# Optimization experiments

Measured on AMD Instinct MI355X. Metric: run time of the kernel, lower is better.

Reference implementation:

```python
import jax, jax.numpy as jnp
import numpy as np

B, T, H, DK, DV, HID, C = 2, 4096, 16, 128, 128, 2048, 64  # chunk size 64 (fla default)
EPS = 1e-5


def setup_inputs() -> dict:
    key = jax.random.key(0)
    ks = jax.random.split(key, 8)
    s = 0.02
    return dict(
        hidden_ab=jax.random.normal(ks[0], (B, T, HID), jnp.float32),
        hidden_g=jax.random.normal(ks[1], (B, T, HID), jnp.float32),
        q=jax.random.normal(ks[2], (B, T, H, DK), jnp.float32),
        k=jax.random.normal(ks[3], (B, T, H, DK), jnp.float32),
        v=jax.random.normal(ks[4], (B, T, H, DV), jnp.float32),
        Wb=jax.random.normal(ks[5], (HID, H), jnp.float32) * s,
        Wg=jax.random.normal(ks[6], (HID, H), jnp.float32) * s,
        o_norm_w=jnp.ones((DV,), jnp.float32),
        o_proj_w=jax.random.normal(ks[7], (H, DV, DK), jnp.float32) * s,
    )


def _l2norm(x):
    return x * jax.lax.rsqrt(jnp.sum(x * x, -1, keepdims=True) + 1e-6)


def reference(hidden_ab, hidden_g, q, k, v, Wb, Wg, o_norm_w, o_proj_w):
    # beta gate per head (training path: sigmoid(b_proj(hidden_ab)))
    beta = jax.nn.sigmoid(hidden_ab @ Wb)  # [B,T,H]
    # qk_norm == 'l2' -> l2 normalization inside the kernel, q scaled by dk^-0.5
    q = _l2norm(q)
    k = _l2norm(k)
    scale = DK ** -0.5
    N = T // C

    def toc(x, d):  # [B,T,H,d] -> [N,B,H,C,d]
        return x.reshape(B, N, C, H, d).transpose(1, 0, 3, 2, 4)

    qc = toc(q * scale, DK)
    kc = toc(k, DK)
    vc = toc(v, DV)
    bc = beta.reshape(B, N, C, H).transpose(1, 0, 3, 2)  # [N,B,H,C]

    k_beta = kc * bc[..., None]
    v_beta = vc * bc[..., None]

    # intra-chunk UT transform: Tm = (I + strict_lower(k_beta k^T))^{-1}
    Lm = jnp.tril(jnp.einsum('nbhik,nbhjk->nbhij', k_beta, kc), -1)  # [N,B,H,C,C]
    eye = jnp.eye(C, dtype=q.dtype)
    Tm = jax.scipy.linalg.solve_triangular(eye + Lm, jnp.broadcast_to(eye, Lm.shape), lower=True)
    u = Tm @ v_beta   # [N,B,H,C,DV]
    w = Tm @ k_beta   # [N,B,H,C,DK]
    attn = jnp.tril(jnp.einsum('nbhik,nbhjk->nbhij', qc, kc))  # causal intra-chunk scores

    def step(S, ins):  # S: [B,H,DK,DV] carried state
        qn, kn, an, un, wn = ins
        vi = un - wn @ S                                   # corrected values
        on = qn @ S + an @ vi                              # inter + intra chunk output
        S = S + jnp.einsum('bhck,bhcv->bhkv', kn, vi)      # state update
        return S, on

    S0 = jnp.zeros((B, H, DK, DV), q.dtype)
    _, o = jax.lax.scan(step, S0, (qc, kc, attn, u, w))    # o: [N,B,H,C,DV]
    o = o.transpose(1, 0, 3, 2, 4).reshape(B, T, H, DV)

    # FusedRMSNormSwishGate with per-head scalar gate broadcast over DV
    g = hidden_g @ Wg  # [B,T,H]
    o = o * jax.lax.rsqrt(jnp.mean(o * o, -1, keepdims=True) + EPS) * o_norm_w
    o = o * (g * jax.nn.sigmoid(g))[..., None]

    # GroupLinear: per-head DV -> head_dim projection, then flatten heads
    out = jnp.einsum('bthv,hvd->bthd', o, o_proj_w).reshape(B, T, H * DK)
    return out
```

## Files before the change

kernel.cpp:

```cpp
#include <hip/hip_runtime.h>
#include <hip/hip_bf16.h>

#define BB 2
#define TT 4096
#define HH 16
#define DKk 128
#define DVv 128
#define HIDD 2048
#define CC 64
#define NN 64
#define GG 8
#define QSCALE 0.08838834764831845f

static __device__ __forceinline__ unsigned short f2bf(float f) {
  unsigned u = __float_as_uint(f);
  u += 0x7fffu + ((u >> 16) & 1u);
  return (unsigned short)(u >> 16);
}
static __device__ __forceinline__ float bf2f(unsigned short s) {
  return __uint_as_float(((unsigned)s) << 16);
}

static __device__ __forceinline__ void barrier_lds_only() {
  asm volatile("s_waitcnt lgkmcnt(0)\n\ts_barrier" ::: "memory");
}

typedef short bf8 __attribute__((ext_vector_type(8)));
typedef float f4 __attribute__((ext_vector_type(4)));

__global__ __launch_bounds__(256) void k0_wt(
    const float* __restrict__ Wb, const float* __restrict__ Wg,
    unsigned short* __restrict__ Wtb, unsigned short* __restrict__ Wtg) {
  int blk = blockIdx.x;
  const float* W = (blk < 8) ? Wb : Wg;
  unsigned short* Wt = (blk < 8) ? Wtb : Wtg;
  int k0 = (blk & 7) * 256;
  int tid = threadIdx.x;
  __shared__ unsigned short st[16][272];
  const float* p = W + (size_t)(k0 + tid) * HH;
#pragma unroll
  for (int h4 = 0; h4 < 4; h4++) {
    float4 x = *(const float4*)(p + h4 * 4);
    st[h4 * 4 + 0][tid] = f2bf(x.x);
    st[h4 * 4 + 1][tid] = f2bf(x.y);
    st[h4 * 4 + 2][tid] = f2bf(x.z);
    st[h4 * 4 + 3][tid] = f2bf(x.w);
  }
  __syncthreads();
  int h = tid >> 4, c = (tid & 15) << 4;
#pragma unroll
  for (int j = 0; j < 16; j++)
    Wt[(size_t)h * HIDD + k0 + c + j] = st[h][c + j];
}

__global__ __launch_bounds__(256) void k1_beta_g(
    const float* __restrict__ hab, const float* __restrict__ hg,
    const unsigned short* __restrict__ Wtb, const unsigned short* __restrict__ Wtg,
    float* __restrict__ beta, float* __restrict__ graw) {
  int tile = blockIdx.x;
  int tid = threadIdx.x;
  int w = tid >> 6, lane = tid & 63;
  int proj = w >> 1, ks = w & 1;
  int n16 = lane & 15, qd = lane >> 4;
  const float* hid = proj ? hg : hab;
  const unsigned short* Wt = proj ? Wtg : Wtb;
  size_t rowbase = (size_t)(tile * 16 + n16) * HIDD;
  int k0 = ks * 1024;

  f4 acc = {0.f, 0.f, 0.f, 0.f};
  for (int s = 0; s < 32; s++) {
    int kk = k0 + s * 32 + qd * 8;
    const float* hp = hid + rowbase + kk;
    float4 h0 = *(const float4*)hp;
    float4 h1 = *(const float4*)(hp + 4);
    bf8 a;
    a[0] = (short)f2bf(h0.x); a[1] = (short)f2bf(h0.y);
    a[2] = (short)f2bf(h0.z); a[3] = (short)f2bf(h0.w);
    a[4] = (short)f2bf(h1.x); a[5] = (short)f2bf(h1.y);
    a[6] = (short)f2bf(h1.z); a[7] = (short)f2bf(h1.w);
    bf8 b = *(const bf8*)&Wt[(size_t)n16 * HIDD + kk];
    acc = __builtin_amdgcn_mfma_f32_16x16x32_bf16(a, b, acc, 0, 0, 0);
  }

  __shared__ float red[2][16][17];
  if (ks == 1) {
#pragma unroll
    for (int r = 0; r < 4; r++) red[proj][qd * 4 + r][n16] = acc[r];
  }
  __syncthreads();
  if (ks == 0) {
#pragma unroll
    for (int r = 0; r < 4; r++) {
      float s = acc[r] + red[proj][qd * 4 + r][n16];
      size_t t = (size_t)(tile * 16 + qd * 4 + r) * HH + n16;
      if (proj == 0) beta[t] = 1.f / (1.f + expf(-s));
      else           graw[t] = s;
    }
  }
}

__global__ __launch_bounds__(256) void k2_l2norm(
    const float* __restrict__ q, const float* __restrict__ k,
    unsigned short* __restrict__ qn, unsigned short* __restrict__ kn) {
  int lane = threadIdx.x & 63, wave = threadIdx.x >> 6;
  for (int u = 0; u < 2; u++) {
    int vec = blockIdx.x * 8 + wave * 2 + u;
    size_t off = (size_t)vec * 64 + lane;
    float2 q2 = ((const float2*)q)[off];
    float2 k2 = ((const float2*)k)[off];
    float sq = q2.x * q2.x + q2.y * q2.y;
    float sk = k2.x * k2.x + k2.y * k2.y;
#pragma unroll
    for (int m = 32; m; m >>= 1) { sq += __shfl_xor(sq, m); sk += __shfl_xor(sk, m); }
    float rq = rsqrtf(sq + 1e-6f) * QSCALE;
    float rk = rsqrtf(sk + 1e-6f);
    unsigned pq = (unsigned)f2bf(q2.x * rq) | ((unsigned)f2bf(q2.y * rq) << 16);
    unsigned pk = (unsigned)f2bf(k2.x * rk) | ((unsigned)f2bf(k2.y * rk) << 16);
    ((unsigned*)qn)[off] = pq;
    ((unsigned*)kn)[off] = pk;
  }
}

#define SW 72
#define K3_M0R 8704
#define K3_M0T 13312
#define K3_M1R 17920
#define K3_M1T 22528
#define K3_TB  27136
#define K3_ARENA 31744

__global__ __launch_bounds__(256) void k3_chunk(
    const unsigned short* __restrict__ qn, const unsigned short* __restrict__ kn,
    const float* __restrict__ beta,
    unsigned short* __restrict__ ATg, unsigned short* __restrict__ Ktg) {
  int cid = blockIdx.x;
  int n = cid & (NN - 1);
  int bh = cid / NN;
  int h = bh & (HH - 1);
  int b = bh / HH;
  int tid = threadIdx.x;
  int w = tid >> 6;
  int lane = tid & 63;
  int n16 = lane & 15;
  int qd = lane >> 4;
  int r0 = w * 16;

  __shared__ __align__(16) unsigned short arena[K3_ARENA];
  __shared__ float sb[CC];
  unsigned short* sk = arena;
  unsigned short* sq = arena + 8704;

  int t0 = n * CC;
#pragma unroll
  for (int p = 0; p < 4; p++) {
    int id = p * 256 + tid, row = id >> 4, c8 = (id & 15) << 3;
    size_t g = ((size_t)((b * TT + t0 + row) * HH + h)) * DKk + c8;
    *(uint4*)&sk[row * 136 + c8] = *(const uint4*)(kn + g);
    *(uint4*)&sq[row * 136 + c8] = *(const uint4*)(qn + g);
  }
  if (tid < CC) sb[tid] = beta[(size_t)((b * TT + t0 + tid) * HH + h)];
  __syncthreads();

  f4 at[4], mk[4];
#pragma unroll
  for (int ct = 0; ct < 4; ct++) { at[ct] = (f4){0,0,0,0}; mk[ct] = (f4){0,0,0,0}; }
#pragma unroll
  for (int s = 0; s < 4; s++) {
    bf8 aq = *(const bf8*)&sq[(r0 + n16) * 136 + s * 32 + qd * 8];
    bf8 ak = *(const bf8*)&sk[(r0 + n16) * 136 + s * 32 + qd * 8];
#pragma unroll
    for (int ct = 0; ct < 4; ct++) {
      bf8 bk = *(const bf8*)&sk[(ct * 16 + n16) * 136 + s * 32 + qd * 8];
      at[ct] = __builtin_amdgcn_mfma_f32_16x16x32_bf16(aq, bk, at[ct], 0, 0, 0);
      mk[ct] = __builtin_amdgcn_mfma_f32_16x16x32_bf16(ak, bk, mk[ct], 0, 0, 0);
    }
  }

  f4 tf[4];
  float mpv[4][4];
#pragma unroll
  for (int ct = 0; ct < 4; ct++) {
#pragma unroll
    for (int r = 0; r < 4; r++) {
      int i = r0 + qd * 4 + r, j = ct * 16 + n16;
      at[ct][r] = (j <= i) ? at[ct][r] : 0.f;
      float mp = (j < i) ? -sb[i] * mk[ct][r] : 0.f;
      mpv[ct][r] = mp;
      tf[ct][r] = (i == j) ? 1.f : mp;
    }
  }
  __syncthreads();

#pragma unroll
  for (int ct = 0; ct < 4; ct++) {
#pragma unroll
    for (int r = 0; r < 4; r++) {
      int i = r0 + qd * 4 + r, j = ct * 16 + n16;
      unsigned short hm = f2bf(mpv[ct][r]);
      arena[K3_M0R + i * SW + j] = hm;
      arena[K3_M0T + j * SW + i] = hm;
      arena[K3_TB + j * SW + i] = f2bf(tf[ct][r]);
    }
  }
  __syncthreads();

  int p = 0;
  for (int it = 1; it <= 5; it++) {
    int mrp = p ? K3_M1R : K3_M0R, mtp = p ? K3_M1T : K3_M0T;
    int mrn = p ? K3_M0R : K3_M1R, mtn = p ? K3_M0T : K3_M1T;
    f4 nr[4];
#pragma unroll
    for (int ct = 0; ct < 4; ct++) nr[ct] = (f4){0,0,0,0};
#pragma unroll
    for (int s = 0; s < 2; s++) {
      bf8 a = *(const bf8*)&arena[mrp + (r0 + n16) * SW + s * 32 + qd * 8];
#pragma unroll
      for (int ct = 0; ct < 4; ct++) {
        bf8 bb = *(const bf8*)&arena[mtp + (ct * 16 + n16) * SW + s * 32 + qd * 8];
        nr[ct] = __builtin_amdgcn_mfma_f32_16x16x32_bf16(a, bb, nr[ct], 0, 0, 0);
      }
    }
#pragma unroll
    for (int ct = 0; ct < 4; ct++) {
#pragma unroll
      for (int r = 0; r < 4; r++) {
        int i = r0 + qd * 4 + r, j = ct * 16 + n16;
        unsigned short hm = f2bf(nr[ct][r]);
        arena[mrn + i * SW + j] = hm;
        arena[mtn + j * SW + i] = hm;
      }
    }
    __syncthreads();

#pragma unroll
    for (int s = 0; s < 2; s++) {
      bf8 a = *(const bf8*)&arena[mrn + (r0 + n16) * SW + s * 32 + qd * 8];
#pragma unroll
      for (int ct = 0; ct < 4; ct++) {
        bf8 bb = *(const bf8*)&arena[K3_TB + (ct * 16 + n16) * SW + s * 32 + qd * 8];
        tf[ct] = __builtin_amdgcn_mfma_f32_16x16x32_bf16(a, bb, tf[ct], 0, 0, 0);
      }
    }
    __syncthreads();

    if (it < 5) {
#pragma unroll
      for (int ct = 0; ct < 4; ct++) {
#pragma unroll
        for (int r = 0; r < 4; r++) {
          int i = r0 + qd * 4 + r, j = ct * 16 + n16;
          arena[K3_TB + j * SW + i] = f2bf(tf[ct][r]);
        }
      }
    }
    p = 1 - p;
  }

#pragma unroll
  for (int ct = 0; ct < 4; ct++) {
#pragma unroll
    for (int r = 0; r < 4; r++) {
      int i = r0 + qd * 4 + r, j = ct * 16 + n16;
      arena[K3_M0R + i * SW + j] = f2bf(at[ct][r]);
      arena[K3_TB + j * SW + i] = f2bf(tf[ct][r]);
    }
  }
  __syncthreads();

  {
    f4 ac[4];
#pragma unroll
    for (int ct = 0; ct < 4; ct++) ac[ct] = (f4){0,0,0,0};
#pragma unroll
    for (int s = 0; s < 2; s++) {
      bf8 a = *(const bf8*)&arena[K3_M0R + (r0 + n16) * SW + s * 32 + qd * 8];
#pragma unroll
      for (int ct = 0; ct < 4; ct++) {
        bf8 bb = *(const bf8*)&arena[K3_TB + (ct * 16 + n16) * SW + s * 32 + qd * 8];
        ac[ct] = __builtin_amdgcn_mfma_f32_16x16x32_bf16(a, bb, ac[ct], 0, 0, 0);
      }
    }
    size_t abase = (size_t)cid * (CC * CC);
#pragma unroll
    for (int ct = 0; ct < 4; ct++)
#pragma unroll
      for (int r = 0; r < 4; r++)
        ATg[abase + (r0 + qd * 4 + r) * CC + ct * 16 + n16] = f2bf(ac[ct][r]);
  }

  {
    size_t kbase = (size_t)cid * (DKk * CC);
#pragma unroll
    for (int t = 0; t < 2; t++) {
      int dkt = w * 32 + t * 16;
      f4 ac[4];
#pragma unroll
      for (int ct = 0; ct < 4; ct++) ac[ct] = (f4){0,0,0,0};
#pragma unroll
      for (int s = 0; s < 2; s++) {
        bf8 a;
#pragma unroll
        for (int jj = 0; jj < 8; jj++)
          a[jj] = (short)sk[(s * 32 + qd * 8 + jj) * 136 + dkt + n16];
#pragma unroll
        for (int ct = 0; ct < 4; ct++) {
          bf8 bb = *(const bf8*)&arena[K3_TB + (ct * 16 + n16) * SW + s * 32 + qd * 8];
          ac[ct] = __builtin_amdgcn_mfma_f32_16x16x32_bf16(a, bb, ac[ct], 0, 0, 0);
        }
      }
#pragma unroll
      for (int ct = 0; ct < 4; ct++)
#pragma unroll
        for (int r = 0; r < 4; r++)
          Ktg[kbase + (dkt + qd * 4 + r) * CC + ct * 16 + n16] = f2bf(ac[ct][r]);
    }
  }
}

__global__ __launch_bounds__(256) void k4_scan(
    const unsigned short* __restrict__ qn, const unsigned short* __restrict__ kn,
    const float* __restrict__ v, const float* __restrict__ beta,
    const unsigned short* __restrict__ ATg, const unsigned short* __restrict__ Ktg,
    float* __restrict__ o) {
  int bi = blockIdx.x;
  int jg = bi >> 5;
  int bh = bi & 31;
  int h = bh & (HH - 1);
  int b = bh >> 4;
  int tid = threadIdx.x;
  int j0 = jg * 16;
  int w = tid >> 6;
  int lane = tid & 63;
  int n16 = lane & 15;
  int qd = lane >> 4;
  int r0 = w * 16;
  int dkbase = w * 32;

  __shared__ __align__(16) unsigned short sk[CC * 136];
  __shared__ __align__(16) unsigned short sq[CC * 136];
  __shared__ __align__(16) unsigned short sSb[16 * 136];
  __shared__ __align__(16) unsigned short sAT[2][CC * SW];
  __shared__ __align__(16) unsigned short sKt[2][DKk * SW];
  __shared__ __align__(16) unsigned short sxT[2][16 * SW];
  __shared__ float sb[CC];

  f4 S0 = {0.f, 0.f, 0.f, 0.f}, S1 = {0.f, 0.f, 0.f, 0.f};
  for (int i = tid; i < 16 * 136; i += 256) sSb[i] = 0;

  int bhBase = (b * HH + h) * NN;

  uint4 pk[4], pq[4], pat[2], pkt[4];
  float4 pv;
  float pb = 0.f;

  {
#pragma unroll
    for (int p = 0; p < 4; p++) {
      int id = p * 256 + tid, row = id >> 4, c8 = (id & 15) << 3;
      size_t g = ((size_t)((b * TT + row) * HH + h)) * DKk + c8;
      pk[p] = *(const uint4*)(kn + g);
      pq[p] = *(const uint4*)(qn + g);
    }
    size_t cb = (size_t)bhBase * (CC * CC);
#pragma unroll
    for (int p = 0; p < 2; p++) {
      int id = p * 256 + tid, row = id >> 3, c8 = (id & 7) << 3;
      pat[p] = *(const uint4*)(ATg + cb + row * CC + c8);
    }
    size_t kb = (size_t)bhBase * (DKk * CC);
#pragma unroll
    for (int p = 0; p < 4; p++) {
      int id = p * 256 + tid, row = id >> 3, c8 = (id & 7) << 3;
      pkt[p] = *(const uint4*)(Ktg + kb + row * CC + c8);
    }
    {
      int c = tid >> 2, c4 = (tid & 3) << 2;
      pv = *(const float4*)(v + ((size_t)((b * TT + c) * HH + h)) * DVv + j0 + c4);
    }
    if (tid < CC) pb = beta[(size_t)((b * TT + tid) * HH + h)];
  }

  for (int n = 0; n < NN; n++) {
    int t0 = n * CC;
    unsigned short* xT = sxT[n & 1];
    unsigned short* aT = sAT[n & 1];
    unsigned short* kT = sKt[n & 1];

#pragma unroll
    for (int p = 0; p < 4; p++) {
      int id = p * 256 + tid, row = id >> 4, c8 = (id & 15) << 3;
      *(uint4*)&sk[row * 136 + c8] = pk[p];
      *(uint4*)&sq[row * 136 + c8] = pq[p];
    }
#pragma unroll
    for (int p = 0; p < 2; p++) {
      int id = p * 256 + tid, row = id >> 3, c8 = (id & 7) << 3;
      *(uint4*)&aT[row * SW + c8] = pat[p];
    }
#pragma unroll
    for (int p = 0; p < 4; p++) {
      int id = p * 256 + tid, row = id >> 3, c8 = (id & 7) << 3;
      *(uint4*)&kT[row * SW + c8] = pkt[p];
    }
    {
      int c = tid >> 2, c4 = (tid & 3) << 2;
      xT[(c4 + 0) * SW + c] = f2bf(pv.x);
      xT[(c4 + 1) * SW + c] = f2bf(pv.y);
      xT[(c4 + 2) * SW + c] = f2bf(pv.z);
      xT[(c4 + 3) * SW + c] = f2bf(pv.w);
    }
    if (tid < CC) sb[tid] = pb;
    barrier_lds_only();

    if (n + 1 < NN) {
      int t0n = t0 + CC;
#pragma unroll
      for (int p = 0; p < 4; p++) {
        int id = p * 256 + tid, row = id >> 4, c8 = (id & 15) << 3;
        size_t g = ((size_t)((b * TT + t0n + row) * HH + h)) * DKk + c8;
        pk[p] = *(const uint4*)(kn + g);
        pq[p] = *(const uint4*)(qn + g);
      }
      size_t cb = (size_t)(bhBase + n + 1) * (CC * CC);
#pragma unroll
      for (int p = 0; p < 2; p++) {
        int id = p * 256 + tid, row = id >> 3, c8 = (id & 7) << 3;
        pat[p] = *(const uint4*)(ATg + cb + row * CC + c8);
      }
      size_t kb = (size_t)(bhBase + n + 1) * (DKk * CC);
#pragma unroll
      for (int p = 0; p < 4; p++) {
        int id = p * 256 + tid, row = id >> 3, c8 = (id & 7) << 3;
        pkt[p] = *(const uint4*)(Ktg + kb + row * CC + c8);
      }
      {
        int c = tid >> 2, c4 = (tid & 3) << 2;
        pv = *(const float4*)(v + ((size_t)((b * TT + t0n + c) * HH + h)) * DVv + j0 + c4);
      }
      if (tid < CC) pb = beta[(size_t)((b * TT + t0n + tid) * HH + h)];
    }

    f4 oacc;
    {
      bf8 bS0 = *(const bf8*)&sSb[n16 * 136 + 0 * 32 + qd * 8];
      bf8 bS1 = *(const bf8*)&sSb[n16 * 136 + 1 * 32 + qd * 8];
      bf8 bS2 = *(const bf8*)&sSb[n16 * 136 + 2 * 32 + qd * 8];
      bf8 bS3 = *(const bf8*)&sSb[n16 * 136 + 3 * 32 + qd * 8];
      bf8 aK0 = *(const bf8*)&sk[(r0 + n16) * 136 + 0 * 32 + qd * 8];
      bf8 aK1 = *(const bf8*)&sk[(r0 + n16) * 136 + 1 * 32 + qd * 8];
      bf8 aK2 = *(const bf8*)&sk[(r0 + n16) * 136 + 2 * 32 + qd * 8];
      bf8 aK3 = *(const bf8*)&sk[(r0 + n16) * 136 + 3 * 32 + qd * 8];
      bf8 aQ0 = *(const bf8*)&sq[(r0 + n16) * 136 + 0 * 32 + qd * 8];
      bf8 aQ1 = *(const bf8*)&sq[(r0 + n16) * 136 + 1 * 32 + qd * 8];
      bf8 aQ2 = *(const bf8*)&sq[(r0 + n16) * 136 + 2 * 32 + qd * 8];
      bf8 aQ3 = *(const bf8*)&sq[(r0 + n16) * 136 + 3 * 32 + qd * 8];
      f4 xa = {0.f, 0.f, 0.f, 0.f}, xc = {0.f, 0.f, 0.f, 0.f};
      f4 oa = {0.f, 0.f, 0.f, 0.f}, ob = {0.f, 0.f, 0.f, 0.f};
      xa = __builtin_amdgcn_mfma_f32_16x16x32_bf16(aK0, bS0, xa, 0, 0, 0);
      xa = __builtin_amdgcn_mfma_f32_16x16x32_bf16(aK1, bS1, xa, 0, 0, 0);
      xc = __builtin_amdgcn_mfma_f32_16x16x32_bf16(aK2, bS2, xc, 0, 0, 0);
      xc = __builtin_amdgcn_mfma_f32_16x16x32_bf16(aK3, bS3, xc, 0, 0, 0);
      oa = __builtin_amdgcn_mfma_f32_16x16x32_bf16(aQ0, bS0, oa, 0, 0, 0);
      oa = __builtin_amdgcn_mfma_f32_16x16x32_bf16(aQ1, bS1, oa, 0, 0, 0);
      ob = __builtin_amdgcn_mfma_f32_16x16x32_bf16(aQ2, bS2, ob, 0, 0, 0);
      ob = __builtin_amdgcn_mfma_f32_16x16x32_bf16(aQ3, bS3, ob, 0, 0, 0);
      oacc = oa + ob;
#pragma unroll
      for (int r = 0; r < 4; r++) {
        int c = r0 + qd * 4 + r;
        float vv = bf2f(xT[n16 * SW + c]);
        xT[n16 * SW + c] = f2bf(sb[c] * (vv - (xa[r] + xc[r])));
      }
    }
    barrier_lds_only();

    {
      bf8 bx0 = *(const bf8*)&xT[n16 * SW + 0 * 32 + qd * 8];
      bf8 bx1 = *(const bf8*)&xT[n16 * SW + 1 * 32 + qd * 8];
      bf8 aA0 = *(const bf8*)&aT[(r0 + n16) * SW + 0 * 32 + qd * 8];
      bf8 aA1 = *(const bf8*)&aT[(r0 + n16) * SW + 1 * 32 + qd * 8];
      oacc = __builtin_amdgcn_mfma_f32_16x16x32_bf16(aA0, bx0, oacc, 0, 0, 0);
      oacc = __builtin_amdgcn_mfma_f32_16x16x32_bf16(aA1, bx1, oacc, 0, 0, 0);
#pragma unroll
      for (int r = 0; r < 4; r++) {
        int c = r0 + qd * 4 + r;
        o[((size_t)((b * TT + t0 + c) * HH + h)) * DVv + j0 + n16] = oacc[r];
      }
      bf8 aT0 = *(const bf8*)&kT[(dkbase + n16) * SW + 0 * 32 + qd * 8];
      bf8 aT1 = *(const bf8*)&kT[(dkbase + n16) * SW + 1 * 32 + qd * 8];
      S0 = __builtin_amdgcn_mfma_f32_16x16x32_bf16(aT0, bx0, S0, 0, 0, 0);
      S0 = __builtin_amdgcn_mfma_f32_16x16x32_bf16(aT1, bx1, S0, 0, 0, 0);
      bf8 aT2 = *(const bf8*)&kT[(dkbase + 16 + n16) * SW + 0 * 32 + qd * 8];
      bf8 aT3 = *(const bf8*)&kT[(dkbase + 16 + n16) * SW + 1 * 32 + qd * 8];
      S1 = __builtin_amdgcn_mfma_f32_16x16x32_bf16(aT2, bx0, S1, 0, 0, 0);
      S1 = __builtin_amdgcn_mfma_f32_16x16x32_bf16(aT3, bx1, S1, 0, 0, 0);
#pragma unroll
      for (int r = 0; r < 4; r++) {
        sSb[n16 * 136 + dkbase + qd * 4 + r] = f2bf(S0[r]);
        sSb[n16 * 136 + dkbase + 16 + qd * 4 + r] = f2bf(S1[r]);
      }
    }
  }
}

__global__ __launch_bounds__(256) void k5_out(
    const float* __restrict__ graw, const float* __restrict__ onw,
    const float* __restrict__ opw, float* __restrict__ out) {
  int bi = blockIdx.x;
  int h = bi & (HH - 1);
  int tt = (bi >> 4) & 127;
  int b = bi >> 11;
  int t0 = tt * 32;
  int tid = threadIdx.x;

  __shared__ __align__(16) unsigned short sP[DVv * DKk];
  __shared__ __align__(16) float so[32 * 129];
  __shared__ float smul[32];
  __shared__ float snw[DVv];

  const float* P = opw + (size_t)h * DVv * DKk;
  for (int r = 0; r < 16; r++) {
    int idx4 = r * 256 + tid;
    float4 pvv = *(const float4*)(P + ((size_t)idx4 << 2));
    unsigned p0 = (unsigned)f2bf(pvv.x) | ((unsigned)f2bf(pvv.y) << 16);
    unsigned p1 = (unsigned)f2bf(pvv.z) | ((unsigned)f2bf(pvv.w) << 16);
    *(uint2*)&sP[idx4 << 2] = make_uint2(p0, p1);
  }
  for (int r = 0; r < 16; r++) {
    int idx = r * 256 + tid;
    int t = idx >> 7, d = idx & 127;
    so[t * 129 + d] = out[((size_t)((b * TT + t0 + t) * HH + h)) * DVv + d];
  }
  if (tid < DVv) snw[tid] = onw[tid];
  __syncthreads();

  {
    int t = tid >> 3, l8 = tid & 7;
    float ss = 0.f;
    for (int j = 0; j < 16; j++) { float x = so[t * 129 + l8 + (j << 3)]; ss += x * x; }
    ss += __shfl_down(ss, 4, 8);
    ss += __shfl_down(ss, 2, 8);
    ss += __shfl_down(ss, 1, 8);
    if (l8 == 0) {
      float rms = rsqrtf(ss * (1.f / 128.f) + 1e-5f);
      float gv = graw[(size_t)((b * TT + t0 + t) * HH + h)];
      float sig = 1.f / (1.f + expf(-gv));
      smul[t] = rms * gv * sig;
    }
  }
  __syncthreads();
  for (int r = 0; r < 16; r++) {
    int idx = r * 256 + tid;
    int t = idx >> 7, d = idx & 127;
    so[t * 129 + d] *= smul[t] * snw[d];
  }
  __syncthreads();

  {
    int ttile = tid >> 5;
    int dt = tid & 31;
    int tb = ttile << 2;
    int d0 = dt << 2;
    float acc[4][4];
#pragma unroll
    for (int a = 0; a < 4; a++)
#pragma unroll
      for (int e = 0; e < 4; e++) acc[a][e] = 0.f;
    for (int vv = 0; vv < DVv; vv++) {
      uint2 u = *(const uint2*)&sP[vv * DKk + d0];
      float p0 = __uint_as_float(u.x << 16);
      float p1 = __uint_as_float(u.x & 0xffff0000u);
      float p2 = __uint_as_float(u.y << 16);
      float p3 = __uint_as_float(u.y & 0xffff0000u);
#pragma unroll
      for (int a = 0; a < 4; a++) {
        float ov = so[(tb + a) * 129 + vv];
        acc[a][0] += ov * p0; acc[a][1] += ov * p1; acc[a][2] += ov * p2; acc[a][3] += ov * p3;
      }
    }
#pragma unroll
    for (int a = 0; a < 4; a++) {
      size_t go = ((size_t)((b * TT + t0 + tb + a) * HH + h)) * DKk + d0;
      float4 r; r.x = acc[a][0]; r.y = acc[a][1]; r.z = acc[a][2]; r.w = acc[a][3];
      *(float4*)(out + go) = r;
    }
  }
}

extern "C" void kernel_launch(void* const* d_in, const int* in_sizes, int n_in,
                              void* d_out, int out_size, void* d_ws, size_t ws_size,
                              hipStream_t stream) {
  (void)in_sizes; (void)n_in; (void)out_size; (void)ws_size;
  const float* hab = (const float*)d_in[0];
  const float* hg  = (const float*)d_in[1];
  const float* q   = (const float*)d_in[2];
  const float* k   = (const float*)d_in[3];
  const float* v   = (const float*)d_in[4];
  const float* Wb  = (const float*)d_in[5];
  const float* Wg  = (const float*)d_in[6];
  const float* onw = (const float*)d_in[7];
  const float* opw = (const float*)d_in[8];
  float* out = (float*)d_out;

  char* ws = (char*)d_ws;
  float* beta          = (float*)(ws);
  float* graw          = (float*)(ws + 524288);
  unsigned short* qn   = (unsigned short*)(ws + 1048576);
  unsigned short* kn   = (unsigned short*)(ws + 34603008);
  unsigned short* ATg  = (unsigned short*)(ws + 68157440);
  unsigned short* Ktg  = (unsigned short*)(ws + 84934656);
  unsigned short* Wtb  = (unsigned short*)(ws + 118489088);
  unsigned short* Wtg  = (unsigned short*)(ws + 118554624);

  hipLaunchKernelGGL(k0_wt, dim3(16), dim3(256), 0, stream,
                     Wb, Wg, Wtb, Wtg);
  hipLaunchKernelGGL(k1_beta_g, dim3(TT * BB / 16), dim3(256), 0, stream,
                     hab, hg, Wtb, Wtg, beta, graw);
  hipLaunchKernelGGL(k2_l2norm, dim3(BB * TT * HH / 8), dim3(256), 0, stream,
                     q, k, qn, kn);
  hipLaunchKernelGGL(k3_chunk, dim3(BB * HH * NN), dim3(256), 0, stream,
                     qn, kn, beta, ATg, Ktg);
  hipLaunchKernelGGL(k4_scan, dim3(BB * HH * GG), dim3(256), 0, stream,
                     qn, kn, v, beta, ATg, Ktg, out);
  hipLaunchKernelGGL(k5_out, dim3(BB * (TT / 32) * HH), dim3(256), 0, stream,
                     graw, onw, opw, out);
}
```

Measured before the change: 611.0 us.

## Load scan operands directly into MFMA registers and use MFMA for output projection

The scan kernel stops staging k, q, AT and Kt chunks through shared memory. Each lane now prefetches its own MFMA fragments straight from global memory into registers, double-buffered across two chunk bodies, which removes most LDS traffic and barriers on the serial per-chunk path. The output-projection kernel swaps its scalar FMA loop for bf16 MFMA, using a weight matrix that a new small kernel pre-transposes to bf16. The cost is higher register pressure in the scan, now pinned at one block per CU, plus an extra launch and workspace buffer.

```diff
diff --git a/kernel.cpp b/kernel.cpp
--- a/kernel.cpp
+++ b/kernel.cpp
@@ -51,6 +51,33 @@
 #pragma unroll
   for (int j = 0; j < 16; j++)
     Wt[(size_t)h * HIDD + k0 + c + j] = st[h][c + j];
+}
+
+__global__ __launch_bounds__(256) void k0p_pt(
+    const float* __restrict__ opw, unsigned short* __restrict__ Ppt) {
+  int h = blockIdx.x;
+  int tid = threadIdx.x;
+  __shared__ unsigned short sp[128 * 132];
+  const float* P = opw + (size_t)h * (DVv * DKk);
+  for (int it = 0; it < 16; it++) {
+    int idx = it * 256 + tid;
+    int vv = idx >> 5, d4 = (idx & 31) << 2;
+    float4 x = *(const float4*)(P + vv * 128 + d4);
+    sp[vv * 132 + d4 + 0] = f2bf(x.x);
+    sp[vv * 132 + d4 + 1] = f2bf(x.y);
+    sp[vv * 132 + d4 + 2] = f2bf(x.z);
+    sp[vv * 132 + d4 + 3] = f2bf(x.w);
+  }
+  __syncthreads();
+  unsigned short* dst = Ppt + (size_t)h * (DVv * DKk);
+  for (int it = 0; it < 8; it++) {
+    int idx = it * 256 + tid;
+    int d = idx >> 4, v8 = (idx & 15) << 3;
+    unsigned short tmp[8];
+#pragma unroll
+    for (int j = 0; j < 8; j++) tmp[j] = sp[(v8 + j) * 132 + d];
+    *(uint4*)&dst[d * 128 + v8] = *(uint4*)tmp;
+  }
 }
 
 __global__ __launch_bounds__(256) void k1_beta_g(
@@ -317,7 +344,112 @@
   }
 }
 
-__global__ __launch_bounds__(256) void k4_scan(
+struct K4Frag {
+  bf8 k0, k1, k2, k3;
+  bf8 q0, q1, q2, q3;
+  bf8 a0, a1;
+  bf8 t0, t1, t2, t3;
+  float4 vv;
+  float b0, b1, b2, b3;
+};
+
+static __device__ __forceinline__ void k4_prefetch(
+    K4Frag& F, int n,
+    const unsigned short* knb, const unsigned short* qnb,
+    const unsigned short* atb, const unsigned short* ktb,
+    const float* vb, const float* bb) {
+  const unsigned short* kp = knb + (size_t)n * (CC * HH * DKk);
+  F.k0 = *(const bf8*)(kp);
+  F.k1 = *(const bf8*)(kp + 32);
+  F.k2 = *(const bf8*)(kp + 64);
+  F.k3 = *(const bf8*)(kp + 96);
+  const unsigned short* qp = qnb + (size_t)n * (CC * HH * DKk);
+  F.q0 = *(const bf8*)(qp);
+  F.q1 = *(const bf8*)(qp + 32);
+  F.q2 = *(const bf8*)(qp + 64);
+  F.q3 = *(const bf8*)(qp + 96);
+  const unsigned short* ap = atb + (size_t)n * (CC * CC);
+  F.a0 = *(const bf8*)(ap);
+  F.a1 = *(const bf8*)(ap + 32);
+  const unsigned short* tp = ktb + (size_t)n * (DKk * CC);
+  F.t0 = *(const bf8*)(tp);
+  F.t1 = *(const bf8*)(tp + 32);
+  F.t2 = *(const bf8*)(tp + 1024);
+  F.t3 = *(const bf8*)(tp + 1024 + 32);
+  F.vv = *(const float4*)(vb + (size_t)n * (CC * HH * DVv));
+  const float* bp = bb + (size_t)n * (CC * HH);
+  F.b0 = bp[0]; F.b1 = bp[HH]; F.b2 = bp[2 * HH]; F.b3 = bp[3 * HH];
+}
+
+static __device__ __forceinline__ void k4_body(
+    const K4Frag& F, K4Frag& FN, int n, bool pf,
+    f4& S0, f4& S1,
+    unsigned short* xT, unsigned short* sSb,
+    float* opn,
+    int n16, int qd, int r0, int dkbase,
+    const unsigned short* knb, const unsigned short* qnb,
+    const unsigned short* atb, const unsigned short* ktb,
+    const float* vb, const float* bb) {
+  if (pf) k4_prefetch(FN, n + 1, knb, qnb, atb, ktb, vb, bb);
+
+  {
+    int col = r0 + n16;
+    xT[(qd * 4 + 0) * SW + col] = f2bf(F.vv.x);
+    xT[(qd * 4 + 1) * SW + col] = f2bf(F.vv.y);
+    xT[(qd * 4 + 2) * SW + col] = f2bf(F.vv.z);
+    xT[(qd * 4 + 3) * SW + col] = f2bf(F.vv.w);
+  }
+  barrier_lds_only();
+
+  f4 oacc;
+  {
+    bf8 bS0 = *(const bf8*)&sSb[n16 * 136 + 0 + qd * 8];
+    bf8 bS1 = *(const bf8*)&sSb[n16 * 136 + 32 + qd * 8];
+    bf8 bS2 = *(const bf8*)&sSb[n16 * 136 + 64 + qd * 8];
+    bf8 bS3 = *(const bf8*)&sSb[n16 * 136 + 96 + qd * 8];
+    f4 xa = {0.f, 0.f, 0.f, 0.f}, xc = {0.f, 0.f, 0.f, 0.f};
+    f4 oa = {0.f, 0.f, 0.f, 0.f}, ob = {0.f, 0.f, 0.f, 0.f};
+    xa = __builtin_amdgcn_mfma_f32_16x16x32_bf16(F.k0, bS0, xa, 0, 0, 0);
+    xa = __builtin_amdgcn_mfma_f32_16x16x32_bf16(F.k1, bS1, xa, 0, 0, 0);
+    xc = __builtin_amdgcn_mfma_f32_16x16x32_bf16(F.k2, bS2, xc, 0, 0, 0);
+    xc = __builtin_amdgcn_mfma_f32_16x16x32_bf16(F.k3, bS3, xc, 0, 0, 0);
+    oa = __builtin_amdgcn_mfma_f32_16x16x32_bf16(F.q0, bS0, oa, 0, 0, 0);
+    oa = __builtin_amdgcn_mfma_f32_16x16x32_bf16(F.q1, bS1, oa, 0, 0, 0);
+    ob = __builtin_amdgcn_mfma_f32_16x16x32_bf16(F.q2, bS2, ob, 0, 0, 0);
+    ob = __builtin_amdgcn_mfma_f32_16x16x32_bf16(F.q3, bS3, ob, 0, 0, 0);
+    oacc = oa + ob;
+    float bv[4] = {F.b0, F.b1, F.b2, F.b3};
+#pragma unroll
+    for (int r = 0; r < 4; r++) {
+      int c = r0 + qd * 4 + r;
+      float vval = bf2f(xT[n16 * SW + c]);
+      xT[n16 * SW + c] = f2bf(bv[r] * (vval - (xa[r] + xc[r])));
+    }
+  }
+  barrier_lds_only();
+
+  {
+    bf8 bx0 = *(const bf8*)&xT[n16 * SW + qd * 8];
+    bf8 bx1 = *(const bf8*)&xT[n16 * SW + 32 + qd * 8];
+    oacc = __builtin_amdgcn_mfma_f32_16x16x32_bf16(F.a0, bx0, oacc, 0, 0, 0);
+    oacc = __builtin_amdgcn_mfma_f32_16x16x32_bf16(F.a1, bx1, oacc, 0, 0, 0);
+#pragma unroll
+    for (int r = 0; r < 4; r++) opn[r * (HH * DVv)] = oacc[r];
+    S0 = __builtin_amdgcn_mfma_f32_16x16x32_bf16(F.t0, bx0, S0, 0, 0, 0);
+    S0 = __builtin_amdgcn_mfma_f32_16x16x32_bf16(F.t1, bx1, S0, 0, 0, 0);
+    S1 = __builtin_amdgcn_mfma_f32_16x16x32_bf16(F.t2, bx0, S1, 0, 0, 0);
+    S1 = __builtin_amdgcn_mfma_f32_16x16x32_bf16(F.t3, bx1, S1, 0, 0, 0);
+    uint2 w0, w1;
+    w0.x = (unsigned)f2bf(S0[0]) | ((unsigned)f2bf(S0[1]) << 16);
+    w0.y = (unsigned)f2bf(S0[2]) | ((unsigned)f2bf(S0[3]) << 16);
+    w1.x = (unsigned)f2bf(S1[0]) | ((unsigned)f2bf(S1[1]) << 16);
+    w1.y = (unsigned)f2bf(S1[2]) | ((unsigned)f2bf(S1[3]) << 16);
+    *(uint2*)&sSb[n16 * 136 + dkbase + qd * 4] = w0;
+    *(uint2*)&sSb[n16 * 136 + dkbase + 16 + qd * 4] = w1;
+  }
+}
+
+__global__ __launch_bounds__(256, 1) void k4_scan(
     const unsigned short* __restrict__ qn, const unsigned short* __restrict__ kn,
     const float* __restrict__ v, const float* __restrict__ beta,
     const unsigned short* __restrict__ ATg, const unsigned short* __restrict__ Ktg,
@@ -336,200 +468,60 @@
   int r0 = w * 16;
   int dkbase = w * 32;
 
-  __shared__ __align__(16) unsigned short sk[CC * 136];
-  __shared__ __align__(16) unsigned short sq[CC * 136];
   __shared__ __align__(16) unsigned short sSb[16 * 136];
-  __shared__ __align__(16) unsigned short sAT[2][CC * SW];
-  __shared__ __align__(16) unsigned short sKt[2][DKk * SW];
   __shared__ __align__(16) unsigned short sxT[2][16 * SW];
-  __shared__ float sb[CC];
 
   f4 S0 = {0.f, 0.f, 0.f, 0.f}, S1 = {0.f, 0.f, 0.f, 0.f};
   for (int i = tid; i < 16 * 136; i += 256) sSb[i] = 0;
 
-  int bhBase = (b * HH + h) * NN;
-
-  uint4 pk[4], pq[4], pat[2], pkt[4];
-  float4 pv;
-  float pb = 0.f;
-
-  {
-#pragma unroll
-    for (int p = 0; p < 4; p++) {
-      int id = p * 256 + tid, row = id >> 4, c8 = (id & 15) << 3;
-      size_t g = ((size_t)((b * TT + row) * HH + h)) * DKk + c8;
-      pk[p] = *(const uint4*)(kn + g);
-      pq[p] = *(const uint4*)(qn + g);
-    }
-    size_t cb = (size_t)bhBase * (CC * CC);
-#pragma unroll
-    for (int p = 0; p < 2; p++) {
-      int id = p * 256 + tid, row = id >> 3, c8 = (id & 7) << 3;
-      pat[p] = *(const uint4*)(ATg + cb + row * CC + c8);
-    }
-    size_t kb = (size_t)bhBase * (DKk * CC);
-#pragma unroll
-    for (int p = 0; p < 4; p++) {
-      int id = p * 256 + tid, row = id >> 3, c8 = (id & 7) << 3;
-      pkt[p] = *(const uint4*)(Ktg + kb + row * CC + c8);
-    }
-    {
-      int c = tid >> 2, c4 = (tid & 3) << 2;
-      pv = *(const float4*)(v + ((size_t)((b * TT + c) * HH + h)) * DVv + j0 + c4);
-    }
-    if (tid < CC) pb = beta[(size_t)((b * TT + tid) * HH + h)];
-  }
-
-  for (int n = 0; n < NN; n++) {
-    int t0 = n * CC;
-    unsigned short* xT = sxT[n & 1];
-    unsigned short* aT = sAT[n & 1];
-    unsigned short* kT = sKt[n & 1];
-
-#pragma unroll
-    for (int p = 0; p < 4; p++) {
-      int id = p * 256 + tid, row = id >> 4, c8 = (id & 15) << 3;
-      *(uint4*)&sk[row * 136 + c8] = pk[p];
-      *(uint4*)&sq[row * 136 + c8] = pq[p];
-    }
-#pragma unroll
-    for (int p = 0; p < 2; p++) {
-      int id = p * 256 + tid, row = id >> 3, c8 = (id & 7) << 3;
-      *(uint4*)&aT[row * SW + c8] = pat[p];
-    }
-#pragma unroll
-    for (int p = 0; p < 4; p++) {
-      int id = p * 256 + tid, row = id >> 3, c8 = (id & 7) << 3;
-      *(uint4*)&kT[row * SW + c8] = pkt[p];
-    }
-    {
-      int c = tid >> 2, c4 = (tid & 3) << 2;
-      xT[(c4 + 0) * SW + c] = f2bf(pv.x);
-      xT[(c4 + 1) * SW + c] = f2bf(pv.y);
-      xT[(c4 + 2) * SW + c] = f2bf(pv.z);
-      xT[(c4 + 3) * SW + c] = f2bf(pv.w);
-    }
-    if (tid < CC) sb[tid] = pb;
-    barrier_lds_only();
-
-    if (n + 1 < NN) {
-      int t0n = t0 + CC;
-#pragma unroll
-      for (int p = 0; p < 4; p++) {
-        int id = p * 256 + tid, row = id >> 4, c8 = (id & 15) << 3;
-        size_t g = ((size_t)((b * TT + t0n + row) * HH + h)) * DKk + c8;
-        pk[p] = *(const uint4*)(kn + g);
-        pq[p] = *(const uint4*)(qn + g);
-      }
-      size_t cb = (size_t)(bhBase + n + 1) * (CC * CC);
-#pragma unroll
-      for (int p = 0; p < 2; p++) {
-        int id = p * 256 + tid, row = id >> 3, c8 = (id & 7) << 3;
-        pat[p] = *(const uint4*)(ATg + cb + row * CC + c8);
-      }
-      size_t kb = (size_t)(bhBase + n + 1) * (DKk * CC);
-#pragma unroll
-      for (int p = 0; p < 4; p++) {
-        int id = p * 256 + tid, row = id >> 3, c8 = (id & 7) << 3;
-        pkt[p] = *(const uint4*)(Ktg + kb + row * CC + c8);
-      }
-      {
-        int c = tid >> 2, c4 = (tid & 3) << 2;
-        pv = *(const float4*)(v + ((size_t)((b * TT + t0n + c) * HH + h)) * DVv + j0 + c4);
-      }
-      if (tid < CC) pb = beta[(size_t)((b * TT + t0n + tid) * HH + h)];
-    }
-
-    f4 oacc;
-    {
-      bf8 bS0 = *(const bf8*)&sSb[n16 * 136 + 0 * 32 + qd * 8];
-      bf8 bS1 = *(const bf8*)&sSb[n16 * 136 + 1 * 32 + qd * 8];
-      bf8 bS2 = *(const bf8*)&sSb[n16 * 136 + 2 * 32 + qd * 8];
-      bf8 bS3 = *(const bf8*)&sSb[n16 * 136 + 3 * 32 + qd * 8];
-      bf8 aK0 = *(const bf8*)&sk[(r0 + n16) * 136 + 0 * 32 + qd * 8];
-      bf8 aK1 = *(const bf8*)&sk[(r0 + n16) * 136 + 1 * 32 + qd * 8];
-      bf8 aK2 = *(const bf8*)&sk[(r0 + n16) * 136 + 2 * 32 + qd * 8];
-      bf8 aK3 = *(const bf8*)&sk[(r0 + n16) * 136 + 3 * 32 + qd * 8];
-      bf8 aQ0 = *(const bf8*)&sq[(r0 + n16) * 136 + 0 * 32 + qd * 8];
-      bf8 aQ1 = *(const bf8*)&sq[(r0 + n16) * 136 + 1 * 32 + qd * 8];
-      bf8 aQ2 = *(const bf8*)&sq[(r0 + n16) * 136 + 2 * 32 + qd * 8];
-      bf8 aQ3 = *(const bf8*)&sq[(r0 + n16) * 136 + 3 * 32 + qd * 8];
-      f4 xa = {0.f, 0.f, 0.f, 0.f}, xc = {0.f, 0.f, 0.f, 0.f};
-      f4 oa = {0.f, 0.f, 0.f, 0.f}, ob = {0.f, 0.f, 0.f, 0.f};
-      xa = __builtin_amdgcn_mfma_f32_16x16x32_bf16(aK0, bS0, xa, 0, 0, 0);
-      xa = __builtin_amdgcn_mfma_f32_16x16x32_bf16(aK1, bS1, xa, 0, 0, 0);
-      xc = __builtin_amdgcn_mfma_f32_16x16x32_bf16(aK2, bS2, xc, 0, 0, 0);
-      xc = __builtin_amdgcn_mfma_f32_16x16x32_bf16(aK3, bS3, xc, 0, 0, 0);
-      oa = __builtin_amdgcn_mfma_f32_16x16x32_bf16(aQ0, bS0, oa, 0, 0, 0);
-      oa = __builtin_amdgcn_mfma_f32_16x16x32_bf16(aQ1, bS1, oa, 0, 0, 0);
-      ob = __builtin_amdgcn_mfma_f32_16x16x32_bf16(aQ2, bS2, ob, 0, 0, 0);
-      ob = __builtin_amdgcn_mfma_f32_16x16x32_bf16(aQ3, bS3, ob, 0, 0, 0);
-      oacc = oa + ob;
-#pragma unroll
-      for (int r = 0; r < 4; r++) {
-        int c = r0 + qd * 4 + r;
-        float vv = bf2f(xT[n16 * SW + c]);
-        xT[n16 * SW + c] = f2bf(sb[c] * (vv - (xa[r] + xc[r])));
-      }
-    }
-    barrier_lds_only();
-
-    {
-      bf8 bx0 = *(const bf8*)&xT[n16 * SW + 0 * 32 + qd * 8];
-      bf8 bx1 = *(const bf8*)&xT[n16 * SW + 1 * 32 + qd * 8];
-      bf8 aA0 = *(const bf8*)&aT[(r0 + n16) * SW + 0 * 32 + qd * 8];
-      bf8 aA1 = *(const bf8*)&aT[(r0 + n16) * SW + 1 * 32 + qd * 8];
-      oacc = __builtin_amdgcn_mfma_f32_16x16x32_bf16(aA0, bx0, oacc, 0, 0, 0);
-      oacc = __builtin_amdgcn_mfma_f32_16x16x32_bf16(aA1, bx1, oacc, 0, 0, 0);
-#pragma unroll
-      for (int r = 0; r < 4; r++) {
-        int c = r0 + qd * 4 + r;
-        o[((size_t)((b * TT + t0 + c) * HH + h)) * DVv + j0 + n16] = oacc[r];
-      }
-      bf8 aT0 = *(const bf8*)&kT[(dkbase + n16) * SW + 0 * 32 + qd * 8];
-      bf8 aT1 = *(const bf8*)&kT[(dkbase + n16) * SW + 1 * 32 + qd * 8];
-      S0 = __builtin_amdgcn_mfma_f32_16x16x32_bf16(aT0, bx0, S0, 0, 0, 0);
-      S0 = __builtin_amdgcn_mfma_f32_16x16x32_bf16(aT1, bx1, S0, 0, 0, 0);
-      bf8 aT2 = *(const bf8*)&kT[(dkbase + 16 + n16) * SW + 0 * 32 + qd * 8];
-      bf8 aT3 = *(const bf8*)&kT[(dkbase + 16 + n16) * SW + 1 * 32 + qd * 8];
-      S1 = __builtin_amdgcn_mfma_f32_16x16x32_bf16(aT2, bx0, S1, 0, 0, 0);
-      S1 = __builtin_amdgcn_mfma_f32_16x16x32_bf16(aT3, bx1, S1, 0, 0, 0);
-#pragma unroll
-      for (int r = 0; r < 4; r++) {
-        sSb[n16 * 136 + dkbase + qd * 4 + r] = f2bf(S0[r]);
-        sSb[n16 * 136 + dkbase + 16 + qd * 4 + r] = f2bf(S1[r]);
-      }
-    }
+  const unsigned short* knb =
+      kn + ((size_t)((b * TT + r0 + n16) * HH + h)) * DKk + qd * 8;
+  const unsigned short* qnb =
+      qn + ((size_t)((b * TT + r0 + n16) * HH + h)) * DKk + qd * 8;
+  size_t bhN = (size_t)(b * HH + h) * NN;
+  const unsigned short* atb = ATg + bhN * (CC * CC) + (r0 + n16) * 64 + qd * 8;
+  const unsigned short* ktb = Ktg + bhN * (DKk * CC) + (dkbase + n16) * 64 + qd * 8;
+  const float* vb =
+      v + ((size_t)((b * TT + r0 + n16) * HH + h)) * DVv + j0 + qd * 4;
+  const float* bb = beta + (size_t)((b * TT + r0 + qd * 4) * HH + h);
+  float* opb =
+      o + ((size_t)((b * TT + r0 + qd * 4) * HH + h)) * DVv + j0 + n16;
+
+  K4Frag FA, FB;
+  k4_prefetch(FA, 0, knb, qnb, atb, ktb, vb, bb);
+
+  for (int n = 0; n < NN; n += 2) {
+    k4_body(FA, FB, n, true, S0, S1, sxT[0], sSb,
+            opb + (size_t)n * (CC * HH * DVv),
+            n16, qd, r0, dkbase, knb, qnb, atb, ktb, vb, bb);
+    k4_body(FB, FA, n + 1, n + 2 < NN, S0, S1, sxT[1], sSb,
+            opb + (size_t)(n + 1) * (CC * HH * DVv),
+            n16, qd, r0, dkbase, knb, qnb, atb, ktb, vb, bb);
   }
 }
 
 __global__ __launch_bounds__(256) void k5_out(
     const float* __restrict__ graw, const float* __restrict__ onw,
-    const float* __restrict__ opw, float* __restrict__ out) {
+    const unsigned short* __restrict__ Ppt, float* __restrict__ out) {
   int bi = blockIdx.x;
   int h = bi & (HH - 1);
   int tt = (bi >> 4) & 127;
   int b = bi >> 11;
   int t0 = tt * 32;
   int tid = threadIdx.x;
-
-  __shared__ __align__(16) unsigned short sP[DVv * DKk];
-  __shared__ __align__(16) float so[32 * 129];
+  int w = tid >> 6;
+  int lane = tid & 63;
+  int n16 = lane & 15;
+  int qd = lane >> 4;
+
+  __shared__ __align__(16) float so[32 * 132];
   __shared__ float smul[32];
   __shared__ float snw[DVv];
 
-  const float* P = opw + (size_t)h * DVv * DKk;
-  for (int r = 0; r < 16; r++) {
-    int idx4 = r * 256 + tid;
-    float4 pvv = *(const float4*)(P + ((size_t)idx4 << 2));
-    unsigned p0 = (unsigned)f2bf(pvv.x) | ((unsigned)f2bf(pvv.y) << 16);
-    unsigned p1 = (unsigned)f2bf(pvv.z) | ((unsigned)f2bf(pvv.w) << 16);
-    *(uint2*)&sP[idx4 << 2] = make_uint2(p0, p1);
-  }
   for (int r = 0; r < 16; r++) {
     int idx = r * 256 + tid;
     int t = idx >> 7, d = idx & 127;
-    so[t * 129 + d] = out[((size_t)((b * TT + t0 + t) * HH + h)) * DVv + d];
+    so[t * 132 + d] = out[((size_t)((b * TT + t0 + t) * HH + h)) * DVv + d];
   }
   if (tid < DVv) snw[tid] = onw[tid];
   __syncthreads();
@@ -537,7 +529,7 @@
   {
     int t = tid >> 3, l8 = tid & 7;
     float ss = 0.f;
-    for (int j = 0; j < 16; j++) { float x = so[t * 129 + l8 + (j << 3)]; ss += x * x; }
+    for (int j = 0; j < 16; j++) { float x = so[t * 132 + l8 + (j << 3)]; ss += x * x; }
     ss += __shfl_down(ss, 4, 8);
     ss += __shfl_down(ss, 2, 8);
     ss += __shfl_down(ss, 1, 8);
@@ -552,37 +544,42 @@
   for (int r = 0; r < 16; r++) {
     int idx = r * 256 + tid;
     int t = idx >> 7, d = idx & 127;
-    so[t * 129 + d] *= smul[t] * snw[d];
+    so[t * 132 + d] *= smul[t] * snw[d];
   }
   __syncthreads();
 
   {
-    int ttile = tid >> 5;
-    int dt = tid & 31;
-    int tb = ttile << 2;
-    int d0 = dt << 2;
-    float acc[4][4];
-#pragma unroll
-    for (int a = 0; a < 4; a++)
-#pragma unroll
-      for (int e = 0; e < 4; e++) acc[a][e] = 0.f;
-    for (int vv = 0; vv < DVv; vv++) {
-      uint2 u = *(const uint2*)&sP[vv * DKk + d0];
-      float p0 = __uint_as_float(u.x << 16);
-      float p1 = __uint_as_float(u.x & 0xffff0000u);
-      float p2 = __uint_as_float(u.y << 16);
-      float p3 = __uint_as_float(u.y & 0xffff0000u);
-#pragma unroll
-      for (int a = 0; a < 4; a++) {
-        float ov = so[(tb + a) * 129 + vv];
-        acc[a][0] += ov * p0; acc[a][1] += ov * p1; acc[a][2] += ov * p2; acc[a][3] += ov * p3;
-      }
-    }
-#pragma unroll
-    for (int a = 0; a < 4; a++) {
-      size_t go = ((size_t)((b * TT + t0 + tb + a) * HH + h)) * DKk + d0;
-      float4 r; r.x = acc[a][0]; r.y = acc[a][1]; r.z = acc[a][2]; r.w = acc[a][3];
-      *(float4*)(out + go) = r;
+    const unsigned short* Pb = Ppt + (size_t)h * (DVv * DKk);
+    int dt0 = w * 2;
+#pragma unroll
+    for (int m = 0; m < 2; m++) {
+      bf8 A[4];
+#pragma unroll
+      for (int ks = 0; ks < 4; ks++) {
+        const float* sp = &so[(m * 16 + n16) * 132 + ks * 32 + qd * 8];
+        float4 f0 = *(const float4*)sp;
+        float4 f1 = *(const float4*)(sp + 4);
+        A[ks][0] = (short)f2bf(f0.x); A[ks][1] = (short)f2bf(f0.y);
+        A[ks][2] = (short)f2bf(f0.z); A[ks][3] = (short)f2bf(f0.w);
+        A[ks][4] = (short)f2bf(f1.x); A[ks][5] = (short)f2bf(f1.y);
+        A[ks][6] = (short)f2bf(f1.z); A[ks][7] = (short)f2bf(f1.w);
+      }
+#pragma unroll
+      for (int dti = 0; dti < 2; dti++) {
+        int dt = dt0 + dti;
+        f4 acc = {0.f, 0.f, 0.f, 0.f};
+#pragma unroll
+        for (int ks = 0; ks < 4; ks++) {
+          bf8 Bf = *(const bf8*)(Pb + (dt * 16 + n16) * 128 + ks * 32 + qd * 8);
+          acc = __builtin_amdgcn_mfma_f32_16x16x32_bf16(A[ks], Bf, acc, 0, 0, 0);
+        }
+#pragma unroll
+        for (int r = 0; r < 4; r++) {
+          size_t go = ((size_t)(b * TT + t0 + m * 16 + qd * 4 + r)) * (HH * DKk)
+                      + h * DKk + dt * 16 + n16;
+          out[go] = acc[r];
+        }
+      }
     }
   }
 }
@@ -611,9 +608,12 @@
   unsigned short* Ktg  = (unsigned short*)(ws + 84934656);
   unsigned short* Wtb  = (unsigned short*)(ws + 118489088);
   unsigned short* Wtg  = (unsigned short*)(ws + 118554624);
+  unsigned short* Ppt  = (unsigned short*)(ws + 118620160);
 
   hipLaunchKernelGGL(k0_wt, dim3(16), dim3(256), 0, stream,
                      Wb, Wg, Wtb, Wtg);
+  hipLaunchKernelGGL(k0p_pt, dim3(HH), dim3(256), 0, stream,
+                     opw, Ppt);
   hipLaunchKernelGGL(k1_beta_g, dim3(TT * BB / 16), dim3(256), 0, stream,
                      hab, hg, Wtb, Wtg, beta, graw);
   hipLaunchKernelGGL(k2_l2norm, dim3(BB * TT * HH / 8), dim3(256), 0, stream,
@@ -623,5 +623,5 @@
   hipLaunchKernelGGL(k4_scan, dim3(BB * HH * GG), dim3(256), 0, stream,
                      qn, kn, v, beta, ATg, Ktg, out);
   hipLaunchKernelGGL(k5_out, dim3(BB * (TT / 32) * HH), dim3(256), 0, stream,
-                     graw, onw, opw, out);
-}
+                     graw, onw, Ppt, out);
+}
```

Measured after the change: 533.6 us. 1.14x faster.
